# Kernel optimization log

Measured on AMD Instinct MI355X. Metric: run time of the kernel, lower is better.

The kernel has to match this reference:

```python
import jax, jax.numpy as jnp
import numpy as np

# Production-scale dims: MD system with 100 atoms, all-pairs distance descriptors,
# single full-dataset batch of 512 frames (module docstring: single batch, no shuffle).
B = 512            # batch (frames)
A = 100            # n_atoms
P = A * (A - 1) // 2   # n_descriptors = 4950 pairwise distances
NNZ = B * P * 6    # each descriptor touches 2 atoms x 3 dims -> 6 nonzeros per (batch, desc)


def setup_inputs() -> dict:
    key = jax.random.key(0)
    k1, k2 = jax.random.split(key)
    # Structured sparsity pattern: descriptor d = distance(pi[d], pj[d]).
    pi, pj = np.triu_indices(A, 1)                         # [P] each
    atom_pat = np.repeat(np.stack([pi, pj], axis=1).reshape(-1), 3)  # [6P]
    dim_pat = np.tile(np.arange(3), 2 * P)                 # [6P]
    des_pat = np.repeat(np.arange(P), 6)                   # [6P]
    batch_ind = np.repeat(np.arange(B), 6 * P)             # [NNZ]
    des_ind = np.tile(des_pat, B)                          # [NNZ]
    flat_pat = atom_pat * 3 + dim_pat                      # atom*3 + dim, [6P]
    # scatter index == batch*(n_atoms*3) + atom*3 + dim (what _get_scatter_indices computes
    # when every (atom, dim) slot is covered)
    scatter_idx = batch_ind * (A * 3) + np.tile(flat_pat, B)
    x = jax.random.normal(k1, (B, P), dtype=jnp.float32)       # dq/d(descriptors)
    left = jax.random.normal(k2, (NNZ,), dtype=jnp.float32)    # nonzero d(desc)/d(pos)
    return {
        "x": x,
        "left": left,
        "batch_ind": jnp.asarray(batch_ind, dtype=jnp.int32),
        "des_ind": jnp.asarray(des_ind, dtype=jnp.int32),
        "scatter_idx": jnp.asarray(scatter_idx, dtype=jnp.int32),
    }


def reference(x, left, batch_ind, des_ind, scatter_idx):
    # gather: right = x[batch_ind, des_ind]   (SmartDerivatives._create_right)
    right = x[batch_ind, des_ind]              # [NNZ]
    src = left * right                         # [NNZ]
    # scatter_sum over flat (batch, atom, dim) slots, then square (chain-rule combine)
    out = jax.ops.segment_sum(src, scatter_idx, num_segments=B * A * 3)
    return jnp.square(out).reshape(B, A * 3)
```

## Files before the change

kernel.cpp:

```cpp
#include <hip/hip_runtime.h>
#include <hip/hip_fp16.h>

#define NB   512
#define NP   4950
#define NG   2475
#define NOUT 300
#define LDC  128
#define BT   1024

__device__ __forceinline__ int rowOf(int p) {
    int i = (int)((199.0f - sqrtf((float)(39601 - 8 * p))) * 0.5f);
    while ((i + 1) * (199 - (i + 1)) / 2 <= p) ++i;
    while (i * (199 - i) / 2 > p) --i;
    return i;
}

__device__ __forceinline__ int a16(int r, int c) {
    return r * LDC + (c ^ (((r >> 1) & 31) << 1));
}

__global__ __launch_bounds__(BT, 8)
void smartderiv_f16(const float* __restrict__ x,
                    const float* __restrict__ left,
                    float* __restrict__ out)
{
    __shared__ __half T3[3][100 * LDC];

    const int b   = blockIdx.x;
    const int tid = threadIdx.x;

    if (tid < 300) {
        const int d = tid / 100, r = tid - 100 * d;
        T3[d][a16(r, r)] = __float2half(0.0f);
    }

    const float*  lb  = left + (size_t)b * (6 * NP);
    const float2* xb2 = (const float2*)(x + (size_t)b * NP);

    for (int g = tid; g < NG; g += BT) {
        const float4* lp = (const float4*)(lb + 12 * g);
        const float4 l0 = lp[0];
        const float4 l1 = lp[1];
        const float4 l2 = lp[2];
        const float2 xv = xb2[g];

        const int p0 = 2 * g;
        const int i0 = rowOf(p0);
        const int j0 = p0 - i0 * (199 - i0) / 2 + i0 + 1;
        int i1, j1;
        if (j0 < 99) { i1 = i0;     j1 = j0 + 1; }
        else         { i1 = i0 + 1; j1 = i1 + 1; }

        T3[0][a16(i0, j0)] = __float2half(l0.x * xv.x);
        T3[1][a16(i0, j0)] = __float2half(l0.y * xv.x);
        T3[2][a16(i0, j0)] = __float2half(l0.z * xv.x);
        T3[0][a16(j0, i0)] = __float2half(l0.w * xv.x);
        T3[1][a16(j0, i0)] = __float2half(l1.x * xv.x);
        T3[2][a16(j0, i0)] = __float2half(l1.y * xv.x);
        T3[0][a16(i1, j1)] = __float2half(l1.z * xv.y);
        T3[1][a16(i1, j1)] = __float2half(l1.w * xv.y);
        T3[2][a16(i1, j1)] = __float2half(l2.x * xv.y);
        T3[0][a16(j1, i1)] = __float2half(l2.y * xv.y);
        T3[1][a16(j1, i1)] = __float2half(l2.z * xv.y);
        T3[2][a16(j1, i1)] = __float2half(l2.w * xv.y);
    }
    __syncthreads();

    if (tid < 600 && tid < 300) { }
    if (tid < 300) {
        const int d = tid / 100;
        const int r = tid - 100 * d;
        const int s = (r >> 1) & 31;
        const __half2* row = (const __half2*)(&T3[d][r * LDC]);

        float acc = 0.0f;
        #pragma unroll
        for (int t = 0; t < 50; ++t) {
            const float2 v = __half22float2(row[t ^ s]);
            acc += v.x + v.y;
        }
        out[(size_t)b * NOUT + r * 3 + d] = acc * acc;
    }
}

extern "C" void kernel_launch(void* const* d_in, const int* in_sizes, int n_in,
                              void* d_out, int out_size, void* d_ws, size_t ws_size,
                              hipStream_t stream) {
    const float* x    = (const float*)d_in[0];
    const float* left = (const float*)d_in[1];
    float* out = (float*)d_out;

    smartderiv_f16<<<NB, BT, 0, stream>>>(x, left, out);
}
```

Baseline: 16.96 us.

## Hoist all group loads before shared-memory writes and split row reduction across two threads

Replaces the strided grid-stride loop with a per-wavefront contiguous partition of the 2475 groups. Each thread now issues all of its global loads (two or three groups) up front, before any shared-memory writes, so that memory latency overlaps. The final row reduction uses 600 threads, with each pair summing half the row and combining through a shuffle, which halves the serial chain per thread. This costs more live registers at 1024 threads per block, and uneven per-wave work since the last 64-chunk is partial.

```diff
diff --git a/kernel.cpp b/kernel.cpp
--- a/kernel.cpp
+++ b/kernel.cpp
@@ -19,10 +19,52 @@
     return r * LDC + (c ^ (((r >> 1) & 31) << 1));
 }
 
+struct GrpL {
+    float4 l0, l1, l2;
+    float2 xv;
+};
+
+__device__ __forceinline__ GrpL loadGrp(const float* __restrict__ lb,
+                                        const float2* __restrict__ xb2, int g) {
+    GrpL G;
+    const float4* lp = (const float4*)(lb + 12 * g);
+    G.l0 = lp[0];
+    G.l1 = lp[1];
+    G.l2 = lp[2];
+    G.xv = xb2[g];
+    return G;
+}
+
+__device__ __forceinline__ void writeGrp(__half* __restrict__ T0,
+                                         __half* __restrict__ T1,
+                                         __half* __restrict__ T2,
+                                         const GrpL& G, int g) {
+    const int p0 = 2 * g;
+    const int i0 = rowOf(p0);
+    const int j0 = p0 - i0 * (199 - i0) / 2 + i0 + 1;
+    int i1, j1;
+    if (j0 < 99) { i1 = i0;     j1 = j0 + 1; }
+    else         { i1 = i0 + 1; j1 = i1 + 1; }
+
+    T0[a16(i0, j0)] = __float2half(G.l0.x * G.xv.x);
+    T1[a16(i0, j0)] = __float2half(G.l0.y * G.xv.x);
+    T2[a16(i0, j0)] = __float2half(G.l0.z * G.xv.x);
+    T0[a16(j0, i0)] = __float2half(G.l0.w * G.xv.x);
+    T1[a16(j0, i0)] = __float2half(G.l1.x * G.xv.x);
+    T2[a16(j0, i0)] = __float2half(G.l1.y * G.xv.x);
+
+    T0[a16(i1, j1)] = __float2half(G.l1.z * G.xv.y);
+    T1[a16(i1, j1)] = __float2half(G.l1.w * G.xv.y);
+    T2[a16(i1, j1)] = __float2half(G.l2.x * G.xv.y);
+    T0[a16(j1, i1)] = __float2half(G.l2.y * G.xv.y);
+    T1[a16(j1, i1)] = __float2half(G.l2.z * G.xv.y);
+    T2[a16(j1, i1)] = __float2half(G.l2.w * G.xv.y);
+}
+
 __global__ __launch_bounds__(BT, 8)
-void smartderiv_f16(const float* __restrict__ x,
-                    const float* __restrict__ left,
-                    float* __restrict__ out)
+void smartderiv_hoist(const float* __restrict__ x,
+                      const float* __restrict__ left,
+                      float* __restrict__ out)
 {
     __shared__ __half T3[3][100 * LDC];
 
@@ -37,49 +79,46 @@
     const float*  lb  = left + (size_t)b * (6 * NP);
     const float2* xb2 = (const float2*)(x + (size_t)b * NP);
 
-    for (int g = tid; g < NG; g += BT) {
-        const float4* lp = (const float4*)(lb + 12 * g);
-        const float4 l0 = lp[0];
-        const float4 l1 = lp[1];
-        const float4 l2 = lp[2];
-        const float2 xv = xb2[g];
+    const int w = tid >> 6, l = tid & 63;
+    const int base = (NG * w) >> 4;
+    const int nw   = ((NG * (w + 1)) >> 4) - base;
+    const int g0 = base + l;
+    const int g1 = base + 64 + l;
+    const int g2 = base + 128 + l;
+    const bool has2 = (128 + l) < nw;
 
-        const int p0 = 2 * g;
-        const int i0 = rowOf(p0);
-        const int j0 = p0 - i0 * (199 - i0) / 2 + i0 + 1;
-        int i1, j1;
-        if (j0 < 99) { i1 = i0;     j1 = j0 + 1; }
-        else         { i1 = i0 + 1; j1 = i1 + 1; }
+    GrpL A = loadGrp(lb, xb2, g0);
+    GrpL B = loadGrp(lb, xb2, g1);
+    GrpL C;
+    if (has2) C = loadGrp(lb, xb2, g2);
 
-        T3[0][a16(i0, j0)] = __float2half(l0.x * xv.x);
-        T3[1][a16(i0, j0)] = __float2half(l0.y * xv.x);
-        T3[2][a16(i0, j0)] = __float2half(l0.z * xv.x);
-        T3[0][a16(j0, i0)] = __float2half(l0.w * xv.x);
-        T3[1][a16(j0, i0)] = __float2half(l1.x * xv.x);
-        T3[2][a16(j0, i0)] = __float2half(l1.y * xv.x);
-        T3[0][a16(i1, j1)] = __float2half(l1.z * xv.y);
-        T3[1][a16(i1, j1)] = __float2half(l1.w * xv.y);
-        T3[2][a16(i1, j1)] = __float2half(l2.x * xv.y);
-        T3[0][a16(j1, i1)] = __float2half(l2.y * xv.y);
-        T3[1][a16(j1, i1)] = __float2half(l2.z * xv.y);
-        T3[2][a16(j1, i1)] = __float2half(l2.w * xv.y);
-    }
+    __half* T0 = T3[0];
+    __half* T1 = T3[1];
+    __half* T2 = T3[2];
+    writeGrp(T0, T1, T2, A, g0);
+    writeGrp(T0, T1, T2, B, g1);
+    if (has2) writeGrp(T0, T1, T2, C, g2);
+
     __syncthreads();
 
-    if (tid < 600 && tid < 300) { }
-    if (tid < 300) {
-        const int d = tid / 100;
-        const int r = tid - 100 * d;
+    if (tid < 600) {
+        const int q = tid >> 1;
+        const int u = tid & 1;
+        const int d = q / 100;
+        const int r = q - 100 * d;
         const int s = (r >> 1) & 31;
         const __half2* row = (const __half2*)(&T3[d][r * LDC]);
 
         float acc = 0.0f;
         #pragma unroll
-        for (int t = 0; t < 50; ++t) {
-            const float2 v = __half22float2(row[t ^ s]);
+        for (int t = 0; t < 25; ++t) {
+            const float2 v = __half22float2(row[(2 * t + u) ^ s]);
             acc += v.x + v.y;
         }
-        out[(size_t)b * NOUT + r * 3 + d] = acc * acc;
+        acc += __shfl_xor(acc, 1);
+        if (u == 0) {
+            out[(size_t)b * NOUT + r * 3 + d] = acc * acc;
+        }
     }
 }
 
@@ -90,5 +129,5 @@
     const float* left = (const float*)d_in[1];
     float* out = (float*)d_out;
 
-    smartderiv_f16<<<NB, BT, 0, stream>>>(x, left, out);
+    smartderiv_hoist<<<NB, BT, 0, stream>>>(x, left, out);
 }
```

Result: slower. 17.86 us (+5.3%).
